# Kernel tuning notes

Measured on AMD Instinct MI355X. Metric: run time of the kernel, lower is better.

The kernel has to match this reference:

```python
import jax, jax.numpy as jnp
import numpy as np

R, K = 16, 64  # rel_size (heads), key_size (head dim)
LN_EPS = 1e-5


def apply_rope(x, pos):
    # pos: [B,S,1,K], halves are sin/cos; x: [B,S,R,K]
    sin, cos = jnp.split(pos, 2, axis=-1)
    x0, x1 = jnp.split(x, 2, axis=-1)
    return jnp.concatenate([x0 * cos - x1 * sin, x0 * sin + x1 * cos], axis=-1)


def setup_inputs() -> dict:
    key = jax.random.key(0)
    ks = jax.random.split(key, 6)
    B, S, H = 2, 2048, 1024
    x = jax.random.normal(ks[0], (B, S, H), dtype=jnp.float32)
    pos = jax.random.uniform(ks[1], (B, S, 1, K), dtype=jnp.float32)
    W_qkv = jax.random.normal(ks[2], (H, R * K * 3), dtype=jnp.float32) * (H ** -0.5)
    b_qkv = jax.random.normal(ks[3], (R * K * 3,), dtype=jnp.float32) * 0.02
    W_out = jax.random.normal(ks[4], (R * K, H), dtype=jnp.float32) * ((R * K) ** -0.5)
    b_out = jax.random.normal(ks[5], (H,), dtype=jnp.float32) * 0.02
    ln_g = jnp.ones((H,), dtype=jnp.float32)
    ln_b = jnp.zeros((H,), dtype=jnp.float32)
    return {"x": x, "pos": pos, "W_qkv": W_qkv, "b_qkv": b_qkv,
            "W_out": W_out, "b_out": b_out, "ln_g": ln_g, "ln_b": ln_b}


def reference(x, pos, W_qkv, b_qkv, W_out, b_out, ln_g, ln_b):
    B, S, H = x.shape
    qkv = (x @ W_qkv + b_qkv).reshape(B, S, R, 3 * K)
    q, k, v = jnp.split(qkv, 3, axis=-1)  # each [B,S,R,K]
    k = k / jnp.linalg.norm(k, axis=-1, keepdims=True)
    q = apply_rope(q, pos)
    k = apply_rope(k, pos)
    # SDPA with scale=1 (as in the original call)
    scores = jnp.einsum('bqhd,bkhd->bhqk', q, k)
    attn = jax.nn.softmax(scores, axis=-1)
    ctx = jnp.einsum('bhqk,bkhd->bqhd', attn, v).reshape(B, S, R * K)
    postx = ctx @ W_out + b_out
    y = x + postx
    mu = jnp.mean(y, axis=-1, keepdims=True)
    var = jnp.mean(jnp.square(y - mu), axis=-1, keepdims=True)
    return (y - mu) * jax.lax.rsqrt(var + LN_EPS) * ln_g + ln_b
```

## Files before the change

kernel.cpp:

```cpp
#include <hip/hip_runtime.h>


#define B_   2
#define S_   2048
#define H_   1024
#define R_   16
#define BS_  (B_*S_)
#define NQKV 3072
#define LOG2E 1.44269504088896f

typedef float    floatx4 __attribute__((ext_vector_type(4)));
typedef _Float16 half8   __attribute__((ext_vector_type(8)));
typedef _Float16 half4   __attribute__((ext_vector_type(4)));
typedef __fp16   fp16x2  __attribute__((ext_vector_type(2)));

#if __has_builtin(__builtin_amdgcn_exp2f)
#define EXP2(x) __builtin_amdgcn_exp2f(x)
#else
#define EXP2(x) exp2f(x)
#endif

__device__ __forceinline__ void gl_lds16(const _Float16* g, _Float16* l) {
    __builtin_amdgcn_global_load_lds(
        (const __attribute__((address_space(1))) unsigned int*)g,
        (__attribute__((address_space(3))) unsigned int*)l, 16, 0, 0);
}

__global__ __launch_bounds__(256) void prep0_kernel(
    const float* __restrict__ x, _Float16* __restrict__ x_h,
    const float* __restrict__ W_qkv, _Float16* __restrict__ wqkv_t,
    const float* __restrict__ W_out, _Float16* __restrict__ wout_t)
{
    __shared__ float tile[32][33];
    int bid = blockIdx.x, tid = threadIdx.x;
    if (bid < 4096) {
        int i = bid * 1024 + tid * 4;
        float4 v = *(const float4*)(x + i);
        half4 h;
        h.x = (_Float16)v.x; h.y = (_Float16)v.y;
        h.z = (_Float16)v.z; h.w = (_Float16)v.w;
        *(half4*)(x_h + i) = h;
        return;
    }
    const float* in; _Float16* out; int rows, cols, bx, by;
    if (bid < 7168) {
        int t = bid - 4096;
        in = W_qkv; out = wqkv_t; rows = H_; cols = NQKV;
        bx = t % 96; by = t / 96;
    } else {
        int t = bid - 7168;
        in = W_out; out = wout_t; rows = H_; cols = H_;
        bx = t & 31; by = t >> 5;
    }
    int cx = bx * 32, ry = by * 32;
    int tx = tid & 31, ty = tid >> 5;
#pragma unroll
    for (int i = 0; i < 32; i += 8)
        tile[ty + i][tx] = in[(size_t)(ry + ty + i) * cols + cx + tx];
    __syncthreads();
#pragma unroll
    for (int i = 0; i < 32; i += 8)
        out[(size_t)(cx + ty + i) * rows + ry + tx] = (_Float16)tile[tx][ty + i];
}

template <bool F16OUT>
__global__ __launch_bounds__(256) void gemm_f16_mfma(
    const _Float16* __restrict__ A, const _Float16* __restrict__ Bt,
    const float* __restrict__ bias, const float* __restrict__ resid,
    float* __restrict__ Cf, _Float16* __restrict__ Ch, int M, int N, int Kd)
{
    __shared__ _Float16 Als[2][4096];
    __shared__ _Float16 Bls[2][4096];
    int tid  = threadIdx.x;
    int lane = tid & 63, w = tid >> 6;
    int wr = w >> 1, wc = w & 1;
    int fr = lane & 15, fq = lane >> 4;
    int m0 = blockIdx.y * 128, n0 = blockIdx.x * 128;

    floatx4 acc[4][4] = {};

    const _Float16* ga[2]; const _Float16* gb[2];
    int loff[2];
#pragma unroll
    for (int i2 = 0; i2 < 2; ++i2) {
        int ch = 2 * w + i2;
        int row = ch * 16 + (lane >> 2), col = (lane & 3) * 8;
        ga[i2] = A  + (size_t)(m0 + row) * Kd + col;
        gb[i2] = Bt + (size_t)(n0 + row) * Kd + col;
        loff[i2] = ch * 512;
    }

    int nIter = Kd >> 5;
#pragma unroll
    for (int i2 = 0; i2 < 2; ++i2) {
        gl_lds16(ga[i2], &Als[0][loff[i2]]);
        gl_lds16(gb[i2], &Bls[0][loff[i2]]);
    }

    for (int it = 0; it < nIter; ++it) {
        int cur = it & 1;
        __syncthreads();
        if (it + 1 < nIter) {
            int k1 = (it + 1) << 5;
#pragma unroll
            for (int i2 = 0; i2 < 2; ++i2) {
                gl_lds16(ga[i2] + k1, &Als[cur ^ 1][loff[i2]]);
                gl_lds16(gb[i2] + k1, &Bls[cur ^ 1][loff[i2]]);
            }
        }
        const _Float16* Ab = Als[cur];
        const _Float16* Bb = Bls[cur];
        half8 af[4], bf[4];
#pragma unroll
        for (int i = 0; i < 4; ++i)
            af[i] = *(const half8*)(Ab + (wr * 64 + i * 16 + fr) * 32 + fq * 8);
#pragma unroll
        for (int j = 0; j < 4; ++j)
            bf[j] = *(const half8*)(Bb + (wc * 64 + j * 16 + fr) * 32 + fq * 8);
#pragma unroll
        for (int i = 0; i < 4; ++i)
#pragma unroll
            for (int j = 0; j < 4; ++j)
                acc[i][j] = __builtin_amdgcn_mfma_f32_16x16x32_f16(
                    af[i], bf[j], acc[i][j], 0, 0, 0);
    }

#pragma unroll
    for (int i = 0; i < 4; ++i)
#pragma unroll
        for (int j = 0; j < 4; ++j)
#pragma unroll
            for (int r2 = 0; r2 < 4; ++r2) {
                int row = m0 + wr * 64 + i * 16 + fq * 4 + r2;
                int col = n0 + wc * 64 + j * 16 + fr;
                float v = acc[i][j][r2] + bias[col];
                if constexpr (F16OUT) {
                    Ch[(size_t)row * N + col] = (_Float16)v;
                } else {
                    if (resid) v += resid[(size_t)row * N + col];
                    Cf[(size_t)row * N + col] = v;
                }
            }
}

__global__ __launch_bounds__(256) void prep1_kernel(
    const _Float16* __restrict__ qkvh, const float* __restrict__ pos,
    _Float16* __restrict__ qt, _Float16* __restrict__ kt,
    _Float16* __restrict__ vt2)
{
    __shared__ float tile[64][65];
    int head = blockIdx.x, tau = blockIdx.y;
    int s0 = tau * 64;
    int b = head >> 4, rh = head & 15;
    int lane = threadIdx.x & 63, w = threadIdx.x >> 6;

#pragma unroll
    for (int si = w; si < 64; si += 4)
        tile[si][lane] =
            (float)qkvh[(size_t)(b * S_ + s0 + si) * NQKV + rh * 192 + 128 + lane];
    __syncthreads();
    {
        int P = lane;
        int op = P >> 3;
        int hi = (P >> 2) & 1, lo = P & 3;
#pragma unroll
        for (int d = w; d < 64; d += 4) {
            int ol = op ^ (d & 7);
            int key = 32 * (ol >> 2) + 16 * hi + 4 * (ol & 3) + lo;
            vt2[(((size_t)head * 32 + tau) * 64 + d) * 64 + P] = (_Float16)tile[key][d];
        }
    }

    for (int i = 0; i < 16; ++i) {
        int s = s0 + w * 16 + i;
        int bs = b * S_ + s;
        const _Float16* base = qkvh + (size_t)bs * NQKV + rh * 192;
        float qv = (float)base[lane];
        float kv = (float)base[64 + lane];

        float ss = kv * kv;
#pragma unroll
        for (int off = 32; off > 0; off >>= 1) ss += __shfl_xor(ss, off);
        kv *= rsqrtf(ss);

        int j = lane & 31;
        float sn = pos[(size_t)bs * 64 + j];
        float cs = pos[(size_t)bs * 64 + 32 + j];
        float qp = __shfl_xor(qv, 32);
        float kp = __shfl_xor(kv, 32);
        float qo, ko;
        if (lane < 32) { qo = qv * cs - qp * sn; ko = kv * cs - kp * sn; }
        else           { qo = qp * sn + qv * cs; ko = kp * sn + kv * cs; }

        size_t oidx = ((size_t)head * S_ + s) * 64 + lane;
        qt[oidx] = (_Float16)(qo * LOG2E);
        kt[oidx] = (_Float16)ko;
    }
}

__global__ __launch_bounds__(256) void attn_mfma_kernel(
    const _Float16* __restrict__ qt, const _Float16* __restrict__ kt,
    const _Float16* __restrict__ vt2, _Float16* __restrict__ ctx)
{
    __shared__ _Float16 Kls[2][4096];
    __shared__ _Float16 Vls[2][4096];

    int head = blockIdx.x, q0 = blockIdx.y * 128;
    int b = head >> 4, rh = head & 15;
    int tid = threadIdx.x, lane = tid & 63, w = tid >> 6;
    int g = lane >> 4, c = lane & 15;

    half8 qf[2][2];
    float mL[2], l_s[2] = {0.f, 0.f};
#pragma unroll
    for (int qg = 0; qg < 2; ++qg) {
        const _Float16* qp =
            qt + ((size_t)head * S_ + q0 + w * 32 + qg * 16 + c) * 64 + 8 * g;
        qf[qg][0] = *(const half8*)qp;
        qf[qg][1] = *(const half8*)(qp + 32);
        float qq = 0.f;
#pragma unroll
        for (int i = 0; i < 8; ++i) {
            float a = (float)qf[qg][0][i], b2 = (float)qf[qg][1][i];
            qq += a * a + b2 * b2;
        }
        qq += __shfl_xor(qq, 16);
        qq += __shfl_xor(qq, 32);
        mL[qg] = sqrtf(qq);
    }

    floatx4 o_acc[2][4] = {};

    const _Float16* kg[2]; const _Float16* vg[2];
    int loff[2];
#pragma unroll
    for (int i2 = 0; i2 < 2; ++i2) {
        int ch = 2 * w + i2;
        int krow = ch * 8 + (lane >> 3);
        int koct = (lane & 7) ^ (lane >> 3);
        kg[i2] = kt + ((size_t)head * S_ + krow) * 64 + koct * 8;
        vg[i2] = vt2 + ((size_t)head * 32) * 4096 + ch * 512 + lane * 8;
        loff[i2] = ch * 512;
    }

    int co = c & 7;

#pragma unroll
    for (int i2 = 0; i2 < 2; ++i2) {
        gl_lds16(kg[i2], &Kls[0][loff[i2]]);
        gl_lds16(vg[i2], &Vls[0][loff[i2]]);
    }

    for (int jt = 0; jt < 32; ++jt) {
        int cur = jt & 1;
        __syncthreads();
        if (jt + 1 < 32) {
#pragma unroll
            for (int i2 = 0; i2 < 2; ++i2) {
                gl_lds16(kg[i2] + (size_t)(jt + 1) * 4096, &Kls[cur ^ 1][loff[i2]]);
                gl_lds16(vg[i2] + (size_t)(jt + 1) * 4096, &Vls[cur ^ 1][loff[i2]]);
            }
        }
        const _Float16* Kbuf = Kls[cur];
        const _Float16* Vbuf = Vls[cur];

        half8 kfr[8];
#pragma unroll
        for (int t = 0; t < 4; ++t) {
            const _Float16* krow = Kbuf + (16 * t + c) * 64;
            kfr[2 * t]     = *(const half8*)(krow + ((g) ^ co) * 8);
            kfr[2 * t + 1] = *(const half8*)(krow + ((4 + g) ^ co) * 8);
        }

        union { half8 v; fp16x2 h2[4]; } pf[2][2];
#pragma unroll
        for (int qg = 0; qg < 2; ++qg) {
            floatx4 sacc[4];
#pragma unroll
            for (int t = 0; t < 4; ++t) {
                floatx4 z = {};
                z = __builtin_amdgcn_mfma_f32_16x16x32_f16(
                    kfr[2 * t], qf[qg][0], z, 0, 0, 0);
                z = __builtin_amdgcn_mfma_f32_16x16x32_f16(
                    kfr[2 * t + 1], qf[qg][1], z, 0, 0, 0);
                sacc[t] = z;
            }
            float mLq = mL[qg], ps = 0.f;
#pragma unroll
            for (int t = 0; t < 4; ++t)
#pragma unroll
                for (int r = 0; r < 4; ++r) {
                    float p = EXP2(sacc[t][r] - mLq);
                    sacc[t][r] = p;
                    ps += p;
                }
            l_s[qg] += ps;
            pf[qg][0].h2[0] = __builtin_amdgcn_cvt_pkrtz(sacc[0][0], sacc[0][1]);
            pf[qg][0].h2[1] = __builtin_amdgcn_cvt_pkrtz(sacc[0][2], sacc[0][3]);
            pf[qg][0].h2[2] = __builtin_amdgcn_cvt_pkrtz(sacc[1][0], sacc[1][1]);
            pf[qg][0].h2[3] = __builtin_amdgcn_cvt_pkrtz(sacc[1][2], sacc[1][3]);
            pf[qg][1].h2[0] = __builtin_amdgcn_cvt_pkrtz(sacc[2][0], sacc[2][1]);
            pf[qg][1].h2[1] = __builtin_amdgcn_cvt_pkrtz(sacc[2][2], sacc[2][3]);
            pf[qg][1].h2[2] = __builtin_amdgcn_cvt_pkrtz(sacc[3][0], sacc[3][1]);
            pf[qg][1].h2[3] = __builtin_amdgcn_cvt_pkrtz(sacc[3][2], sacc[3][3]);
        }

#pragma unroll
        for (int t = 0; t < 4; ++t) {
            const _Float16* vrow = Vbuf + (16 * t + c) * 64;
            half8 v0 = *(const half8*)(vrow + ((g) ^ co) * 8);
            half8 v1 = *(const half8*)(vrow + ((4 + g) ^ co) * 8);
#pragma unroll
            for (int qg = 0; qg < 2; ++qg) {
                o_acc[qg][t] = __builtin_amdgcn_mfma_f32_16x16x32_f16(
                    v0, pf[qg][0].v, o_acc[qg][t], 0, 0, 0);
                o_acc[qg][t] = __builtin_amdgcn_mfma_f32_16x16x32_f16(
                    v1, pf[qg][1].v, o_acc[qg][t], 0, 0, 0);
            }
        }
    }

#pragma unroll
    for (int qg = 0; qg < 2; ++qg) {
        float lt = l_s[qg];
        lt += __shfl_xor(lt, 16);
        lt += __shfl_xor(lt, 32);
        float inv = 1.f / lt;
        size_t rowbase =
            ((size_t)(b * S_ + q0 + w * 32 + qg * 16 + c)) * 1024 + rh * 64;
#pragma unroll
        for (int t = 0; t < 4; ++t) {
            union { half4 v; fp16x2 h2[2]; } e;
            e.h2[0] = __builtin_amdgcn_cvt_pkrtz(o_acc[qg][t][0] * inv,
                                                 o_acc[qg][t][1] * inv);
            e.h2[1] = __builtin_amdgcn_cvt_pkrtz(o_acc[qg][t][2] * inv,
                                                 o_acc[qg][t][3] * inv);
            *(half4*)(ctx + rowbase + 16 * t + 4 * g) = e.v;
        }
    }
}

__global__ __launch_bounds__(256) void ln_kernel(
    float* __restrict__ y, const float* __restrict__ g, const float* __restrict__ bb)
{
    int row = blockIdx.x, tid = threadIdx.x;
    float* p = y + (size_t)row * 1024;
    float4 v = ((const float4*)p)[tid];
    float sum = v.x + v.y + v.z + v.w;
    float sq  = v.x*v.x + v.y*v.y + v.z*v.z + v.w*v.w;
#pragma unroll
    for (int off = 32; off > 0; off >>= 1) {
        sum += __shfl_xor(sum, off);
        sq  += __shfl_xor(sq,  off);
    }
    __shared__ float rs[4], rq[4];
    int w = tid >> 6;
    if ((tid & 63) == 0) { rs[w] = sum; rq[w] = sq; }
    __syncthreads();
    sum = rs[0] + rs[1] + rs[2] + rs[3];
    sq  = rq[0] + rq[1] + rq[2] + rq[3];
    float mean = sum * (1.f / 1024.f);
    float var  = sq * (1.f / 1024.f) - mean * mean;
    float inv  = rsqrtf(var + 1e-5f);
    float4 gv = ((const float4*)g)[tid];
    float4 bv = ((const float4*)bb)[tid];
    v.x = (v.x - mean) * inv * gv.x + bv.x;
    v.y = (v.y - mean) * inv * gv.y + bv.y;
    v.z = (v.z - mean) * inv * gv.z + bv.z;
    v.w = (v.w - mean) * inv * gv.w + bv.w;
    ((float4*)p)[tid] = v;
}

extern "C" void kernel_launch(void* const* d_in, const int* in_sizes, int n_in,
                              void* d_out, int out_size, void* d_ws, size_t ws_size,
                              hipStream_t stream)
{
    const float* x     = (const float*)d_in[0];
    const float* pos   = (const float*)d_in[1];
    const float* W_qkv = (const float*)d_in[2];
    const float* b_qkv = (const float*)d_in[3];
    const float* W_out = (const float*)d_in[4];
    const float* b_out = (const float*)d_in[5];
    const float* ln_g  = (const float*)d_in[6];
    const float* ln_b  = (const float*)d_in[7];
    float* out = (float*)d_out;

    char* ws = (char*)d_ws;
    _Float16* x_h    = (_Float16*)(ws);
    _Float16* wqkv_t = (_Float16*)(ws + ((size_t)8  << 20));
    _Float16* wout_t = (_Float16*)(ws + ((size_t)14 << 20));
    _Float16* qkvh   = (_Float16*)(ws + ((size_t)16 << 20));
    _Float16* qt_h   = (_Float16*)(ws + ((size_t)40 << 20));
    _Float16* kt_h   = (_Float16*)(ws + ((size_t)48 << 20));
    _Float16* vt2_h  = (_Float16*)(ws + ((size_t)56 << 20));
    _Float16* ctx_h  = (_Float16*)(ws + ((size_t)64 << 20));

    prep0_kernel<<<8192, 256, 0, stream>>>(x, x_h, W_qkv, wqkv_t, W_out, wout_t);

    gemm_f16_mfma<true><<<dim3(NQKV / 128, BS_ / 128), 256, 0, stream>>>(
        x_h, wqkv_t, b_qkv, nullptr, nullptr, qkvh, BS_, NQKV, H_);

    prep1_kernel<<<dim3(32, 32), 256, 0, stream>>>(qkvh, pos, qt_h, kt_h, vt2_h);

    attn_mfma_kernel<<<dim3(32, 16), 256, 0, stream>>>(qt_h, kt_h, vt2_h, ctx_h);

    gemm_f16_mfma<false><<<dim3(H_ / 128, BS_ / 128), 256, 0, stream>>>(
        ctx_h, wout_t, b_out, x, out, nullptr, BS_, H_, H_);

    ln_kernel<<<BS_, 256, 0, stream>>>(out, ln_g, ln_b);
}
```

Measured before the change: 228.7 us.

## Split attention over two key halves with merge, use 64x64 tiles for output GEMM

The attention kernel now splits the key range into two halves along a third grid dimension. Each half writes unnormalized partial outputs in fp16 plus row sums, and a new merge kernel adds them and normalizes. This doubles the block count from 512 to 1024 so more of the GPU's compute units are occupied. It relies on the fixed upper-bound max (query norm) already being shared, so no max rescaling is needed. The output projection switches to a new 64x64-tile GEMM, giving 1024 blocks instead of 256 to improve occupancy, at the cost of less data reuse, plus an extra kernel launch and an fp16 round-trip for the partials.

```diff
diff --git a/kernel.cpp b/kernel.cpp
--- a/kernel.cpp
+++ b/kernel.cpp
@@ -63,11 +63,10 @@
         out[(size_t)(cx + ty + i) * rows + ry + tx] = (_Float16)tile[tx][ty + i];
 }
 
-template <bool F16OUT>
 __global__ __launch_bounds__(256) void gemm_f16_mfma(
     const _Float16* __restrict__ A, const _Float16* __restrict__ Bt,
-    const float* __restrict__ bias, const float* __restrict__ resid,
-    float* __restrict__ Cf, _Float16* __restrict__ Ch, int M, int N, int Kd)
+    const float* __restrict__ bias, _Float16* __restrict__ Ch,
+    int M, int N, int Kd)
 {
     __shared__ _Float16 Als[2][4096];
     __shared__ _Float16 Bls[2][4096];
@@ -133,13 +132,68 @@
             for (int r2 = 0; r2 < 4; ++r2) {
                 int row = m0 + wr * 64 + i * 16 + fq * 4 + r2;
                 int col = n0 + wc * 64 + j * 16 + fr;
-                float v = acc[i][j][r2] + bias[col];
-                if constexpr (F16OUT) {
-                    Ch[(size_t)row * N + col] = (_Float16)v;
-                } else {
-                    if (resid) v += resid[(size_t)row * N + col];
-                    Cf[(size_t)row * N + col] = v;
-                }
+                Ch[(size_t)row * N + col] = (_Float16)(acc[i][j][r2] + bias[col]);
+            }
+}
+
+__global__ __launch_bounds__(256) void gemm64_f16_mfma(
+    const _Float16* __restrict__ A, const _Float16* __restrict__ Bt,
+    const float* __restrict__ bias, const float* __restrict__ resid,
+    float* __restrict__ Cf, int M, int N, int Kd)
+{
+    __shared__ _Float16 Als[2][2048];
+    __shared__ _Float16 Bls[2][2048];
+    int tid = threadIdx.x, lane = tid & 63, w = tid >> 6;
+    int wr = w >> 1, wc = w & 1;
+    int fr = lane & 15, fq = lane >> 4;
+    int m0 = blockIdx.y * 64, n0 = blockIdx.x * 64;
+
+    floatx4 acc[2][2] = {};
+
+    int srow = w * 16 + (lane >> 2), scol = (lane & 3) * 8;
+    const _Float16* ga = A  + (size_t)(m0 + srow) * Kd + scol;
+    const _Float16* gb = Bt + (size_t)(n0 + srow) * Kd + scol;
+    int loff = w * 512;
+
+    int nIter = Kd >> 5;
+    gl_lds16(ga, &Als[0][loff]);
+    gl_lds16(gb, &Bls[0][loff]);
+
+    for (int it = 0; it < nIter; ++it) {
+        int cur = it & 1;
+        __syncthreads();
+        if (it + 1 < nIter) {
+            int k1 = (it + 1) << 5;
+            gl_lds16(ga + k1, &Als[cur ^ 1][loff]);
+            gl_lds16(gb + k1, &Bls[cur ^ 1][loff]);
+        }
+        const _Float16* Ab = Als[cur];
+        const _Float16* Bb = Bls[cur];
+        half8 af[2], bf[2];
+#pragma unroll
+        for (int i = 0; i < 2; ++i)
+            af[i] = *(const half8*)(Ab + (wr * 32 + i * 16 + fr) * 32 + fq * 8);
+#pragma unroll
+        for (int j = 0; j < 2; ++j)
+            bf[j] = *(const half8*)(Bb + (wc * 32 + j * 16 + fr) * 32 + fq * 8);
+#pragma unroll
+        for (int i = 0; i < 2; ++i)
+#pragma unroll
+            for (int j = 0; j < 2; ++j)
+                acc[i][j] = __builtin_amdgcn_mfma_f32_16x16x32_f16(
+                    af[i], bf[j], acc[i][j], 0, 0, 0);
+    }
+
+#pragma unroll
+    for (int i = 0; i < 2; ++i)
+#pragma unroll
+        for (int j = 0; j < 2; ++j)
+#pragma unroll
+            for (int r2 = 0; r2 < 4; ++r2) {
+                int row = m0 + wr * 32 + i * 16 + fq * 4 + r2;
+                int col = n0 + wc * 32 + j * 16 + fr;
+                Cf[(size_t)row * N + col] =
+                    acc[i][j][r2] + bias[col] + resid[(size_t)row * N + col];
             }
 }
 
@@ -200,12 +254,13 @@
 
 __global__ __launch_bounds__(256) void attn_mfma_kernel(
     const _Float16* __restrict__ qt, const _Float16* __restrict__ kt,
-    const _Float16* __restrict__ vt2, _Float16* __restrict__ ctx)
+    const _Float16* __restrict__ vt2,
+    _Float16* __restrict__ opart, float* __restrict__ lpart)
 {
     __shared__ _Float16 Kls[2][4096];
     __shared__ _Float16 Vls[2][4096];
 
-    int head = blockIdx.x, q0 = blockIdx.y * 128;
+    int head = blockIdx.x, q0 = blockIdx.y * 128, ks = blockIdx.z;
     int b = head >> 4, rh = head & 15;
     int tid = threadIdx.x, lane = tid & 63, w = tid >> 6;
     int g = lane >> 4, c = lane & 15;
@@ -244,21 +299,23 @@
     }
 
     int co = c & 7;
+    int jbase = ks << 4;
 
 #pragma unroll
     for (int i2 = 0; i2 < 2; ++i2) {
-        gl_lds16(kg[i2], &Kls[0][loff[i2]]);
-        gl_lds16(vg[i2], &Vls[0][loff[i2]]);
-    }
-
-    for (int jt = 0; jt < 32; ++jt) {
+        gl_lds16(kg[i2] + (size_t)jbase * 4096, &Kls[0][loff[i2]]);
+        gl_lds16(vg[i2] + (size_t)jbase * 4096, &Vls[0][loff[i2]]);
+    }
+
+    for (int jt = 0; jt < 16; ++jt) {
         int cur = jt & 1;
         __syncthreads();
-        if (jt + 1 < 32) {
+        if (jt + 1 < 16) {
+            size_t joff = (size_t)(jbase + jt + 1) * 4096;
 #pragma unroll
             for (int i2 = 0; i2 < 2; ++i2) {
-                gl_lds16(kg[i2] + (size_t)(jt + 1) * 4096, &Kls[cur ^ 1][loff[i2]]);
-                gl_lds16(vg[i2] + (size_t)(jt + 1) * 4096, &Vls[cur ^ 1][loff[i2]]);
+                gl_lds16(kg[i2] + joff, &Kls[cur ^ 1][loff[i2]]);
+                gl_lds16(vg[i2] + joff, &Vls[cur ^ 1][loff[i2]]);
             }
         }
         const _Float16* Kbuf = Kls[cur];
@@ -325,19 +382,43 @@
         float lt = l_s[qg];
         lt += __shfl_xor(lt, 16);
         lt += __shfl_xor(lt, 32);
-        float inv = 1.f / lt;
+        int q = q0 + w * 32 + qg * 16 + c;
+        if (lane < 16)
+            lpart[((size_t)ks * 32 + head) * S_ + q] = lt;
         size_t rowbase =
-            ((size_t)(b * S_ + q0 + w * 32 + qg * 16 + c)) * 1024 + rh * 64;
+            ((size_t)ks * BS_ + (size_t)(b * S_ + q)) * 1024 + rh * 64;
 #pragma unroll
         for (int t = 0; t < 4; ++t) {
             union { half4 v; fp16x2 h2[2]; } e;
-            e.h2[0] = __builtin_amdgcn_cvt_pkrtz(o_acc[qg][t][0] * inv,
-                                                 o_acc[qg][t][1] * inv);
-            e.h2[1] = __builtin_amdgcn_cvt_pkrtz(o_acc[qg][t][2] * inv,
-                                                 o_acc[qg][t][3] * inv);
-            *(half4*)(ctx + rowbase + 16 * t + 4 * g) = e.v;
-        }
-    }
+            e.h2[0] = __builtin_amdgcn_cvt_pkrtz(o_acc[qg][t][0], o_acc[qg][t][1]);
+            e.h2[1] = __builtin_amdgcn_cvt_pkrtz(o_acc[qg][t][2], o_acc[qg][t][3]);
+            *(half4*)(opart + rowbase + 16 * t + 4 * g) = e.v;
+        }
+    }
+}
+
+__global__ __launch_bounds__(256) void merge_kernel(
+    const _Float16* __restrict__ opart, const float* __restrict__ lpart,
+    _Float16* __restrict__ ctx)
+{
+    int idx = blockIdx.x * 256 + threadIdx.x;
+    int row = idx >> 7;
+    int col = (idx & 127) * 8;
+    int b = row >> 11, s = row & 2047;
+    int head = b * 16 + (col >> 6);
+    float l0 = lpart[(size_t)head * S_ + s];
+    float l1 = lpart[(size_t)(32 + head) * S_ + s];
+    float inv = 1.f / (l0 + l1);
+    size_t off = (size_t)row * 1024 + col;
+    half8 a = *(const half8*)(opart + off);
+    half8 b8 = *(const half8*)(opart + (size_t)BS_ * 1024 + off);
+    union { half8 v; fp16x2 h2[4]; } e;
+#pragma unroll
+    for (int i = 0; i < 4; ++i)
+        e.h2[i] = __builtin_amdgcn_cvt_pkrtz(
+            ((float)a[2 * i]     + (float)b8[2 * i])     * inv,
+            ((float)a[2 * i + 1] + (float)b8[2 * i + 1]) * inv);
+    *(half8*)(ctx + off) = e.v;
 }
 
 __global__ __launch_bounds__(256) void ln_kernel(
@@ -394,18 +475,23 @@
     _Float16* kt_h   = (_Float16*)(ws + ((size_t)48 << 20));
     _Float16* vt2_h  = (_Float16*)(ws + ((size_t)56 << 20));
     _Float16* ctx_h  = (_Float16*)(ws + ((size_t)64 << 20));
+    _Float16* opart  = (_Float16*)(ws + ((size_t)72 << 20));
+    float*    lpart  = (float*)   (ws + ((size_t)88 << 20));
 
     prep0_kernel<<<8192, 256, 0, stream>>>(x, x_h, W_qkv, wqkv_t, W_out, wout_t);
 
-    gemm_f16_mfma<true><<<dim3(NQKV / 128, BS_ / 128), 256, 0, stream>>>(
-        x_h, wqkv_t, b_qkv, nullptr, nullptr, qkvh, BS_, NQKV, H_);
+    gemm_f16_mfma<<<dim3(NQKV / 128, BS_ / 128), 256, 0, stream>>>(
+        x_h, wqkv_t, b_qkv, qkvh, BS_, NQKV, H_);
 
     prep1_kernel<<<dim3(32, 32), 256, 0, stream>>>(qkvh, pos, qt_h, kt_h, vt2_h);
 
-    attn_mfma_kernel<<<dim3(32, 16), 256, 0, stream>>>(qt_h, kt_h, vt2_h, ctx_h);
-
-    gemm_f16_mfma<false><<<dim3(H_ / 128, BS_ / 128), 256, 0, stream>>>(
-        ctx_h, wout_t, b_out, x, out, nullptr, BS_, H_, H_);
+    attn_mfma_kernel<<<dim3(32, 16, 2), 256, 0, stream>>>(
+        qt_h, kt_h, vt2_h, opart, lpart);
+
+    merge_kernel<<<2048, 256, 0, stream>>>(opart, lpart, ctx_h);
+
+    gemm64_f16_mfma<<<dim3(H_ / 64, BS_ / 64), 256, 0, stream>>>(
+        ctx_h, wout_t, b_out, x, out, BS_, H_, H_);
 
     ln_kernel<<<BS_, 256, 0, stream>>>(out, ln_g, ln_b);
 }
```

Result: faster. 223.9 us (-2.1%).
